# Optimization experiments

Measured on AMD Instinct MI355X. Metric: run time of the kernel, lower is better.

The kernel has to match this reference:

```python
import jax, jax.numpy as jnp
import numpy as np

B, N, D = 16, 1024, 768
H = 12
HS = D // H
L = 2  # n_ffn_layers
EPS = 1e-6


def layernorm(x, scale, bias):
    mu = jnp.mean(x, axis=-1, keepdims=True)
    var = jnp.var(x, axis=-1, keepdims=True)
    return (x - mu) * jax.lax.rsqrt(var + EPS) * scale + bias


def log_cosh(x):
    # numerically stable log(cosh(x)) = |x| + log1p(exp(-2|x|)) - log(2)
    ax = jnp.abs(x)
    return ax + jnp.log1p(jnp.exp(-2.0 * ax)) - jnp.log(2.0)


def setup_inputs() -> dict:
    key = jax.random.key(0)
    ks = jax.random.split(key, 8)
    x = jax.random.normal(ks[0], (B, N, D), dtype=jnp.float32)
    # pre-attention LayerNorm params
    ln1_scale = jnp.ones((D,), jnp.float32)
    ln1_bias = jnp.zeros((D,), jnp.float32)
    # per-head value projections [H, D, HS] (Dense, no bias)
    Wv = jax.random.normal(ks[1], (H, D, HS), jnp.float32) / np.sqrt(D)
    # per-head circulant rows alpha_delta [H, N], truncated_normal(stddev=sqrt(1/N))
    alpha = jax.random.truncated_normal(ks[2], -2.0, 2.0, (H, N), jnp.float32) * np.sqrt(1.0 / N)
    # FFN: L layers of Dense(D) + LayerNorm + swish
    Wf = jax.random.normal(ks[3], (L, D, D), jnp.float32) / np.sqrt(D)
    bf = jnp.zeros((L, D), jnp.float32)
    lnf_scale = jnp.ones((L, D), jnp.float32)
    lnf_bias = jnp.zeros((L, D), jnp.float32)
    return {"x": x, "ln1_scale": ln1_scale, "ln1_bias": ln1_bias, "Wv": Wv,
            "alpha": alpha, "Wf": Wf, "bf": bf,
            "lnf_scale": lnf_scale, "lnf_bias": lnf_bias}


def reference(x, ln1_scale, ln1_bias, Wv, alpha, Wf, bf, lnf_scale, lnf_bias):
    b, n, d = x.shape
    h, hs = Wv.shape[0], Wv.shape[2]
    # --- multi-head positional (circulant) attention on LN(x) ---
    xn = layernorm(x, ln1_scale, ln1_bias)
    v = jnp.einsum('bnd,hdk->bhnk', xn, Wv)  # per-head values
    # circulant matrix C[h, i, j] = alpha[h, (i - j) mod n]  (scipy.linalg.circulant)
    idx = (jnp.arange(n)[:, None] - jnp.arange(n)[None, :]) % n  # [n, n]
    C = alpha[:, idx]                                            # [h, n, n]
    y = jnp.einsum('hij,bhjk->bhik', C, v)                       # [b, h, n, hs]
    y = jnp.transpose(y, (0, 2, 1, 3)).reshape(b, n, h * hs)     # concat heads
    x = x + y
    # --- FFN: [Dense(D) -> LayerNorm -> swish] x L ---
    z = x
    for l in range(Wf.shape[0]):
        z = jax.nn.swish(layernorm(z @ Wf[l] + bf[l], lnf_scale[l], lnf_bias[l]))
    return log_cosh(z + x)
```

## Files before the change

### kernel.cpp

```cpp
#include <hip/hip_runtime.h>
#include <cstdint>
#include <cstddef>


typedef __attribute__((ext_vector_type(8))) short bf16x8;
typedef __attribute__((ext_vector_type(4))) float f32x4;
typedef __attribute__((ext_vector_type(4))) unsigned short us4;

__device__ __forceinline__ unsigned short f2bf(float f) {
  unsigned int u = __builtin_bit_cast(unsigned int, f);
  u += 0x7FFFu + ((u >> 16) & 1u);
  return (unsigned short)(u >> 16);
}
__device__ __forceinline__ float bf2f(unsigned short u) {
  return __builtin_bit_cast(float, (unsigned int)u << 16);
}

__device__ __forceinline__ void g2l16(const void* g, void* l) {
  __builtin_amdgcn_global_load_lds(
      (const __attribute__((address_space(1))) unsigned int*)g,
      (__attribute__((address_space(3))) unsigned int*)l,
      16, 0, 0);
}

#define BARX asm volatile("s_waitcnt lgkmcnt(0)\n\ts_barrier" ::: "memory")
#define BARV(n) asm volatile("s_waitcnt vmcnt(" #n ") lgkmcnt(0)\n\ts_barrier" ::: "memory")

__global__ __launch_bounds__(256) void pack_all(const float* __restrict__ Wv,
                                                const float* __restrict__ Wf,
                                                unsigned short* __restrict__ W2t,
                                                unsigned short* __restrict__ Wft) {
  int bid = blockIdx.x;
  if (bid < 2304) {
    int o = bid * 256 + threadIdx.x;
    int np = o / 768, d = o - np * 768;
    int h = np >> 6, k = np & 63;
    W2t[o] = f2bf(Wv[h * 49152 + d * 64 + k]);
  } else {
    int o = (bid - 2304) * 256 + threadIdx.x;
    int l = o / 589824, rem = o - l * 589824;
    int np = rem / 768, d = rem - np * 768;
    Wft[o] = f2bf(Wf[l * 589824 + d * 768 + np]);
  }
}

__device__ __forceinline__ void wave_reduce2(float& s, float& s2) {
#pragma unroll
  for (int off = 32; off > 0; off >>= 1) {
    s += __shfl_down(s, off);
    s2 += __shfl_down(s2, off);
  }
  s = __shfl(s, 0);
  s2 = __shfl(s2, 0);
}

__global__ __launch_bounds__(256) void ln1_kernel(const float* __restrict__ x,
                                                  const float* __restrict__ sc,
                                                  const float* __restrict__ bi,
                                                  unsigned short* __restrict__ out) {
  int row = blockIdx.x * 4 + (threadIdx.x >> 6);
  int lane = threadIdx.x & 63;
  size_t base = (size_t)row * 768;
  float4 v[3];
#pragma unroll
  for (int j = 0; j < 3; ++j) v[j] = *(const float4*)(x + base + lane * 4 + j * 256);
  float s = 0.f, s2 = 0.f;
#pragma unroll
  for (int j = 0; j < 3; ++j) {
    s += v[j].x + v[j].y + v[j].z + v[j].w;
    s2 += v[j].x * v[j].x + v[j].y * v[j].y + v[j].z * v[j].z + v[j].w * v[j].w;
  }
  wave_reduce2(s, s2);
  float mu = s * (1.0f / 768.0f);
  float var = s2 * (1.0f / 768.0f) - mu * mu;
  float r = rsqrtf(var + 1e-6f);
#pragma unroll
  for (int j = 0; j < 3; ++j) {
    int d = lane * 4 + j * 256;
    float4 scv = *(const float4*)(sc + d);
    float4 biv = *(const float4*)(bi + d);
    us4 o;
    o[0] = f2bf((v[j].x - mu) * r * scv.x + biv.x);
    o[1] = f2bf((v[j].y - mu) * r * scv.y + biv.y);
    o[2] = f2bf((v[j].z - mu) * r * scv.z + biv.z);
    o[3] = f2bf((v[j].w - mu) * r * scv.w + biv.w);
    *(us4*)(out + base + d) = o;
  }
}

__global__ __launch_bounds__(256) void lnswish_kernel(const unsigned short* __restrict__ g,
                                                      const float* __restrict__ sc,
                                                      const float* __restrict__ bi,
                                                      unsigned short* __restrict__ out) {
  int row = blockIdx.x * 4 + (threadIdx.x >> 6);
  int lane = threadIdx.x & 63;
  size_t base = (size_t)row * 768;
  float v[3][4];
#pragma unroll
  for (int j = 0; j < 3; ++j) {
    us4 gv = *(const us4*)(g + base + lane * 4 + j * 256);
#pragma unroll
    for (int q = 0; q < 4; ++q) v[j][q] = bf2f(gv[q]);
  }
  float s = 0.f, s2 = 0.f;
#pragma unroll
  for (int j = 0; j < 3; ++j)
#pragma unroll
    for (int q = 0; q < 4; ++q) { s += v[j][q]; s2 += v[j][q] * v[j][q]; }
  wave_reduce2(s, s2);
  float mu = s * (1.0f / 768.0f);
  float var = s2 * (1.0f / 768.0f) - mu * mu;
  float r = rsqrtf(var + 1e-6f);
#pragma unroll
  for (int j = 0; j < 3; ++j) {
    int d = lane * 4 + j * 256;
    float4 scv = *(const float4*)(sc + d);
    float4 biv = *(const float4*)(bi + d);
    const float* scp = &scv.x;
    const float* bip = &biv.x;
    us4 o;
#pragma unroll
    for (int q = 0; q < 4; ++q) {
      float z = (v[j][q] - mu) * r * scp[q] + bip[q];
      o[q] = f2bf(z / (1.0f + __expf(-z)));
    }
    *(us4*)(out + base + d) = o;
  }
}

__global__ __launch_bounds__(256) void final_kernel(const unsigned short* __restrict__ g,
                                                    const float* __restrict__ sc,
                                                    const float* __restrict__ bi,
                                                    const unsigned short* __restrict__ x2,
                                                    float* __restrict__ out) {
  int row = blockIdx.x * 4 + (threadIdx.x >> 6);
  int lane = threadIdx.x & 63;
  size_t base = (size_t)row * 768;
  float v[3][4];
#pragma unroll
  for (int j = 0; j < 3; ++j) {
    us4 gv = *(const us4*)(g + base + lane * 4 + j * 256);
#pragma unroll
    for (int q = 0; q < 4; ++q) v[j][q] = bf2f(gv[q]);
  }
  float s = 0.f, s2 = 0.f;
#pragma unroll
  for (int j = 0; j < 3; ++j)
#pragma unroll
    for (int q = 0; q < 4; ++q) { s += v[j][q]; s2 += v[j][q] * v[j][q]; }
  wave_reduce2(s, s2);
  float mu = s * (1.0f / 768.0f);
  float var = s2 * (1.0f / 768.0f) - mu * mu;
  float r = rsqrtf(var + 1e-6f);
#pragma unroll
  for (int j = 0; j < 3; ++j) {
    int d = lane * 4 + j * 256;
    float4 scv = *(const float4*)(sc + d);
    float4 biv = *(const float4*)(bi + d);
    us4 xv = *(const us4*)(x2 + base + d);
    const float* scp = &scv.x;
    const float* bip = &biv.x;
    float4 o;
    float* op = &o.x;
#pragma unroll
    for (int q = 0; q < 4; ++q) {
      float z = (v[j][q] - mu) * r * scp[q] + bip[q];
      float sw = z / (1.0f + __expf(-z));
      float t = sw + bf2f(xv[q]);
      float ax = fabsf(t);
      op[q] = ax + __logf(1.0f + __expf(-2.0f * ax)) - 0.69314718055994531f;
    }
    *(float4*)(out + base + d) = o;
  }
}

template <int K>
__device__ __forceinline__ void gemm256(const unsigned short* __restrict__ A,
                                        const unsigned short* __restrict__ Bt,
                                        int m0, int n0, unsigned short* lds,
                                        f32x4 acc[8][4]) {
  const int tid = threadIdx.x;
  const int lane = tid & 63;
  const int wid = tid >> 6;
  const int wm = (wid >> 2) << 6;
  const int wn = (wid & 3) << 5;
  const int fm = lane & 15, fq = lane >> 4;
  const int srow = tid >> 3;
  const int sslot = (tid & 7) ^ (srow & 7);
  const size_t abase = (size_t)(m0 + srow) * K + (sslot << 3);
  const size_t bbase = (size_t)(n0 + srow) * K + (sslot << 3);

  bf16x8 aq[4][2], bq[4][2];

#define STG_A(kt, bb, c)                                                     \
  g2l16(A + abase + (size_t)((c) << 6) * K + ((kt) << 6),                    \
        lds + ((bb) << 15) + ((c) << 12) + (tid << 3))
#define STG_B(kt, bb, c)                                                     \
  g2l16(Bt + bbase + (size_t)((c) << 6) * K + ((kt) << 6),                   \
        lds + ((bb) << 15) + 16384 + ((c) << 12) + (tid << 3))
#define LDA(bb, mh)                                                          \
  _Pragma("unroll") for (int mt = 0; mt < 4; ++mt) {                         \
    const unsigned short* p =                                                \
        lds + ((bb) << 15) + (wm + ((mh) << 7) + (mt << 4) + fm) * 64;       \
    _Pragma("unroll") for (int kk = 0; kk < 2; ++kk)                         \
      aq[mt][kk] = *(const bf16x8*)(p + ((((kk << 2) + fq) ^ (fm & 7)) << 3)); \
  }
#define LDB(bb, nh)                                                          \
  _Pragma("unroll") for (int nt = 0; nt < 2; ++nt) {                         \
    const unsigned short* p = lds + ((bb) << 15) + 16384 +                   \
                              (wn + ((nh) << 7) + (nt << 4) + fm) * 64;      \
    _Pragma("unroll") for (int kk = 0; kk < 2; ++kk)                         \
      bq[((nh) << 1) + nt][kk] =                                             \
          *(const bf16x8*)(p + ((((kk << 2) + fq) ^ (fm & 7)) << 3));        \
  }
#define MMX(mh, nh)                                                          \
  {                                                                          \
    __builtin_amdgcn_s_setprio(1);                                           \
    _Pragma("unroll") for (int mt = 0; mt < 4; ++mt)                         \
    _Pragma("unroll") for (int nt = 0; nt < 2; ++nt)                         \
    _Pragma("unroll") for (int kk = 0; kk < 2; ++kk)                         \
      acc[((mh) << 2) + mt][((nh) << 1) + nt] =                              \
          __builtin_amdgcn_mfma_f32_16x16x32_bf16(                           \
              aq[mt][kk], bq[((nh) << 1) + nt][kk],                          \
              acc[((mh) << 2) + mt][((nh) << 1) + nt], 0, 0, 0);             \
    __builtin_amdgcn_s_setprio(0);                                           \
  }

  constexpr int NT = K >> 6;
  STG_A(0, 0, 0); STG_A(0, 0, 1); STG_A(0, 0, 2); STG_A(0, 0, 3);
  STG_B(0, 0, 0); STG_B(0, 0, 1); STG_B(0, 0, 2); STG_B(0, 0, 3);
  STG_A(1, 1, 0); STG_A(1, 1, 1);
  STG_B(1, 1, 0); STG_B(1, 1, 1);
  BARV(4);

  for (int t = 0; t < (NT >> 1) - 1; ++t) {
    const int k1 = 2 * t + 1, k2 = 2 * t + 2, k3 = 2 * t + 3;
    LDA(0, 0); LDB(0, 0);
    STG_A(k1, 1, 2); STG_A(k1, 1, 3);
    MMX(0, 0); BARX;
    LDB(0, 1);
    STG_B(k1, 1, 2); STG_B(k1, 1, 3);
    MMX(0, 1); BARX;
    LDA(0, 1);
    STG_A(k2, 0, 0); STG_A(k2, 0, 1);
    MMX(1, 0); BARX;
    STG_B(k2, 0, 0); STG_B(k2, 0, 1);
    MMX(1, 1); BARV(4);
    LDA(1, 0); LDB(1, 0);
    STG_A(k2, 0, 2); STG_A(k2, 0, 3);
    MMX(0, 0); BARX;
    LDB(1, 1);
    STG_B(k2, 0, 2); STG_B(k2, 0, 3);
    MMX(0, 1); BARX;
    LDA(1, 1);
    STG_A(k3, 1, 0); STG_A(k3, 1, 1);
    MMX(1, 0); BARX;
    STG_B(k3, 1, 0); STG_B(k3, 1, 1);
    MMX(1, 1); BARV(4);
  }
  {
    const int k1 = NT - 1;
    LDA(0, 0); LDB(0, 0);
    STG_A(k1, 1, 2); STG_A(k1, 1, 3);
    MMX(0, 0); BARX;
    LDB(0, 1);
    STG_B(k1, 1, 2); STG_B(k1, 1, 3);
    MMX(0, 1); BARX;
    LDA(0, 1);
    MMX(1, 0); BARX;
    MMX(1, 1);
    BARV(0);
    LDA(1, 0); LDB(1, 0);
    MMX(0, 0); BARX;
    LDB(1, 1);
    MMX(0, 1); BARX;
    LDA(1, 1);
    MMX(1, 0); BARX;
    MMX(1, 1);
  }
#undef STG_A
#undef STG_B
#undef LDA
#undef LDB
#undef MMX
}

__device__ __forceinline__ void decode256(int bid, int& m0, int& n0) {
  int wg = (bid & 7) * 24 + (bid >> 3);
  int mi = wg / 3, ni = wg - mi * 3;
  m0 = mi << 8;
  n0 = ni << 8;
}

__global__ __launch_bounds__(512, 2) void gemm1_256(const unsigned short* __restrict__ A,
                                                    const unsigned short* __restrict__ W2t,
                                                    unsigned short* __restrict__ Vt) {
  extern __shared__ unsigned short lds[];
  f32x4 acc[8][4] = {};
  int m0, n0;
  decode256(blockIdx.x, m0, n0);
  gemm256<768>(A, W2t, m0, n0, lds, acc);
  const int lane = threadIdx.x & 63, wid = threadIdx.x >> 6;
  const int wm = (wid >> 2) << 6, wn = (wid & 3) << 5;
  const int fm = lane & 15, fq = lane >> 4;
#pragma unroll
  for (int ai = 0; ai < 8; ++ai) {
    int rowb = m0 + wm + ((ai >> 2) << 7) + ((ai & 3) << 4) + (fq << 2);
    int b = rowb >> 10, n = rowb & 1023;
#pragma unroll
    for (int nj = 0; nj < 4; ++nj) {
      int col = n0 + wn + ((nj >> 1) << 7) + ((nj & 1) << 4) + fm;
      int h = col >> 6, ck = col & 63;
      size_t off = ((size_t)h << 20) + (size_t)((b << 6) + ck) * 1024 + n;
      us4 v;
#pragma unroll
      for (int r = 0; r < 4; ++r) v[r] = f2bf(acc[ai][nj][r]);
      *(us4*)(Vt + off) = v;
    }
  }
}

__global__ __launch_bounds__(512, 2) void gemmf_256(const unsigned short* __restrict__ A,
                                                    const unsigned short* __restrict__ Bt,
                                                    const float* __restrict__ bias,
                                                    unsigned short* __restrict__ g) {
  extern __shared__ unsigned short lds[];
  f32x4 acc[8][4] = {};
  int m0, n0;
  decode256(blockIdx.x, m0, n0);
  gemm256<768>(A, Bt, m0, n0, lds, acc);
  const int lane = threadIdx.x & 63, wid = threadIdx.x >> 6;
  const int wm = (wid >> 2) << 6, wn = (wid & 3) << 5;
  const int fm = lane & 15, fq = lane >> 4;
#pragma unroll
  for (int ai = 0; ai < 8; ++ai) {
    int rowb = m0 + wm + ((ai >> 2) << 7) + ((ai & 3) << 4) + (fq << 2);
#pragma unroll
    for (int nj = 0; nj < 4; ++nj) {
      int col = n0 + wn + ((nj >> 1) << 7) + ((nj & 1) << 4) + fm;
      float bc = bias[col];
#pragma unroll
      for (int r = 0; r < 4; ++r)
        g[(size_t)(rowb + r) * 768 + col] = f2bf(acc[ai][nj][r] + bc);
    }
  }
}

__global__ __launch_bounds__(512, 2) void circ256_kernel(const float* __restrict__ alpha,
                                                         const unsigned short* __restrict__ Vt,
                                                         const float* __restrict__ xin,
                                                         unsigned short* __restrict__ x2bf) {
  extern __shared__ unsigned short lds[];
  unsigned short* sAc = lds;
  unsigned short* sB = lds + 10304;
  f32x4 acc[8][4] = {};

  int wg = (blockIdx.x & 7) * 24 + (blockIdx.x >> 3);
  int h = wg >> 4, tt = wg & 15;
  int m0 = (tt >> 2) << 8, n0 = (tt & 3) << 8;

  const int tid = threadIdx.x;
  const int lane = tid & 63, wid = tid >> 6;
  const int wm = (wid >> 2) << 6, wn = (wid & 3) << 5;
  const int fm = lane & 15, fq = lane >> 4;
  const int srow = tid >> 3;
  const int sslot = (tid & 7) ^ (srow & 7);

  const float* ah = alpha + (h << 10);
#pragma unroll
  for (int c = 0; c < 8; ++c)
    for (int u = tid; u < 1280; u += 512)
      sAc[c * 1288 + u] = f2bf(ah[(m0 - 769 - u - c) & 1023]);

  const unsigned short* Bt = Vt + ((size_t)h << 20);
  const size_t bbase = (size_t)(n0 + srow) * 1024 + (sslot << 3);

  bf16x8 aq[4][2], bq[4][2];

#define CSTG(kt, bb, c)                                                      \
  g2l16(Bt + bbase + (size_t)((c) << 6) * 1024 + ((kt) << 6),                \
        sB + ((bb) << 14) + ((c) << 12) + (tid << 3))
#define CLDA(kt, mh)                                                         \
  _Pragma("unroll") for (int mt = 0; mt < 4; ++mt)                           \
  _Pragma("unroll") for (int kk = 0; kk < 2; ++kk) {                         \
    int d_ = ((kt) << 6) + (kk << 5) + (fq << 3) + 255 -                     \
             (wm + ((mh) << 7) + (mt << 4) + fm);                            \
    int c_ = d_ & 7;                                                         \
    aq[mt][kk] = *(const bf16x8*)(sAc + c_ * 1288 + (d_ - c_));              \
  }
#define CLDB(bb, nh)                                                         \
  _Pragma("unroll") for (int nt = 0; nt < 2; ++nt) {                         \
    const unsigned short* p =                                                \
        sB + ((bb) << 14) + (wn + ((nh) << 7) + (nt << 4) + fm) * 64;        \
    _Pragma("unroll") for (int kk = 0; kk < 2; ++kk)                         \
      bq[((nh) << 1) + nt][kk] =                                             \
          *(const bf16x8*)(p + ((((kk << 2) + fq) ^ (fm & 7)) << 3));        \
  }
#define CMMX(mh, nh)                                                         \
  {                                                                          \
    __builtin_amdgcn_s_setprio(1);                                           \
    _Pragma("unroll") for (int mt = 0; mt < 4; ++mt)                         \
    _Pragma("unroll") for (int nt = 0; nt < 2; ++nt)                         \
    _Pragma("unroll") for (int kk = 0; kk < 2; ++kk)                         \
      acc[((mh) << 2) + mt][((nh) << 1) + nt] =                              \
          __builtin_amdgcn_mfma_f32_16x16x32_bf16(                           \
              aq[mt][kk], bq[((nh) << 1) + nt][kk],                          \
              acc[((mh) << 2) + mt][((nh) << 1) + nt], 0, 0, 0);             \
    __builtin_amdgcn_s_setprio(0);                                           \
  }

  CSTG(0, 0, 0); CSTG(0, 0, 1); CSTG(0, 0, 2); CSTG(0, 0, 3);
  CSTG(1, 1, 0); CSTG(1, 1, 1);
  BARV(2);

  for (int it = 0; it < 7; ++it) {
    const int k0 = 2 * it, k1 = 2 * it + 1, k2 = 2 * it + 2, k3 = 2 * it + 3;
    CLDA(k0, 0); CLDB(0, 0);
    CSTG(k1, 1, 2);
    CMMX(0, 0); BARX;
    CLDB(0, 1);
    CSTG(k1, 1, 3);
    CMMX(0, 1); BARX;
    CLDA(k0, 1);
    CSTG(k2, 0, 0);
    CMMX(1, 0); BARX;
    CSTG(k2, 0, 1);
    CMMX(1, 1); BARV(2);
    CLDA(k1, 0); CLDB(1, 0);
    CSTG(k2, 0, 2);
    CMMX(0, 0); BARX;
    CLDB(1, 1);
    CSTG(k2, 0, 3);
    CMMX(0, 1); BARX;
    CLDA(k1, 1);
    CSTG(k3, 1, 0);
    CMMX(1, 0); BARX;
    CSTG(k3, 1, 1);
    CMMX(1, 1); BARV(2);
  }
  CLDA(14, 0); CLDB(0, 0);
  CSTG(15, 1, 2);
  CMMX(0, 0); BARX;
  CLDB(0, 1);
  CSTG(15, 1, 3);
  CMMX(0, 1); BARX;
  CLDA(14, 1);
  CMMX(1, 0); BARX;
  CMMX(1, 1);
  BARV(0);
  CLDA(15, 0); CLDB(1, 0);
  CMMX(0, 0); BARX;
  CLDB(1, 1);
  CMMX(0, 1); BARX;
  CLDA(15, 1);
  CMMX(1, 0); BARX;
  CMMX(1, 1);
#undef CSTG
#undef CLDA
#undef CLDB
#undef CMMX

#pragma unroll
  for (int ai = 0; ai < 8; ++ai) {
    int i = m0 + wm + ((ai >> 2) << 7) + ((ai & 3) << 4) + (fq << 2);
#pragma unroll
    for (int nj = 0; nj < 4; ++nj) {
      int col = n0 + wn + ((nj >> 1) << 7) + ((nj & 1) << 4) + fm;
      int b = col >> 6, k = col & 63;
      size_t off = ((size_t)(b << 10) + i) * 768 + (h << 6) + k;
#pragma unroll
      for (int r = 0; r < 4; ++r) {
        float val = acc[ai][nj][r] + xin[off + (size_t)r * 768];
        x2bf[off + (size_t)r * 768] = f2bf(val);
      }
    }
  }
}

extern "C" void kernel_launch(void* const* d_in, const int* in_sizes, int n_in,
                              void* d_out, int out_size, void* d_ws, size_t ws_size,
                              hipStream_t stream) {
  const float* x = (const float*)d_in[0];
  const float* ln1_s = (const float*)d_in[1];
  const float* ln1_b = (const float*)d_in[2];
  const float* Wv = (const float*)d_in[3];
  const float* alpha = (const float*)d_in[4];
  const float* Wf = (const float*)d_in[5];
  const float* bf = (const float*)d_in[6];
  const float* lnf_s = (const float*)d_in[7];
  const float* lnf_b = (const float*)d_in[8];
  float* out = (float*)d_out;

  char* ws = (char*)d_ws;
  unsigned short* slotA = (unsigned short*)ws;
  unsigned short* Vt = (unsigned short*)(ws + 25165824);
  unsigned short* gbf = Vt;
  unsigned short* slotX = (unsigned short*)(ws + 50331648);
  unsigned short* W2t = (unsigned short*)(ws + 75497472);
  unsigned short* Wft = (unsigned short*)(ws + 76677120);

  hipFuncSetAttribute((const void*)gemm1_256,
                      hipFuncAttributeMaxDynamicSharedMemorySize, 131072);
  hipFuncSetAttribute((const void*)gemmf_256,
                      hipFuncAttributeMaxDynamicSharedMemorySize, 131072);
  hipFuncSetAttribute((const void*)circ256_kernel,
                      hipFuncAttributeMaxDynamicSharedMemorySize, 86144);

  pack_all<<<6912, 256, 0, stream>>>(Wv, Wf, W2t, Wft);

  ln1_kernel<<<4096, 256, 0, stream>>>(x, ln1_s, ln1_b, slotA);
  gemm1_256<<<192, 512, 131072, stream>>>(slotA, W2t, Vt);
  circ256_kernel<<<192, 512, 86144, stream>>>(alpha, Vt, x, slotX);
  gemmf_256<<<192, 512, 131072, stream>>>(slotX, Wft, bf, gbf);
  lnswish_kernel<<<4096, 256, 0, stream>>>(gbf, lnf_s, lnf_b, slotA);
  gemmf_256<<<192, 512, 131072, stream>>>(slotA, Wft + 589824, bf + 768, gbf);
  final_kernel<<<4096, 256, 0, stream>>>(gbf, lnf_s + 768, lnf_b + 768, slotX, out);
}
```

Before: 270.3 us.

## Fuse second FFN GEMM with LayerNorm, swish, residual and log-cosh epilogue

Replaces the last gemmf_256 plus final_kernel pair with one kernel that computes 64-row by full-768-column output tiles. Owning whole rows lets it do the LayerNorm reduction in-block through shuffles and LDS, then apply swish, the residual add and log_cosh before writing fp32 output. This removes the bf16 round trip of the GEMM result and one launch. In exchange it uses a new 256-block grid with a shallower two-stage pipeline. The epilogue's scalar column-strided stores and residual loads may also coalesce less well.

Result: slower. 277.9 us (+2.8%).

```diff
diff --git a/kernel.cpp b/kernel.cpp
--- a/kernel.cpp
+++ b/kernel.cpp
@@ -23,6 +23,7 @@
       16, 0, 0);
 }
 
+#define WAITB(n) asm volatile("s_waitcnt vmcnt(" #n ") lgkmcnt(0)\n\ts_barrier" ::: "memory")
 #define BARX asm volatile("s_waitcnt lgkmcnt(0)\n\ts_barrier" ::: "memory")
 #define BARV(n) asm volatile("s_waitcnt vmcnt(" #n ") lgkmcnt(0)\n\ts_barrier" ::: "memory")
 
@@ -125,52 +126,6 @@
       o[q] = f2bf(z / (1.0f + __expf(-z)));
     }
     *(us4*)(out + base + d) = o;
-  }
-}
-
-__global__ __launch_bounds__(256) void final_kernel(const unsigned short* __restrict__ g,
-                                                    const float* __restrict__ sc,
-                                                    const float* __restrict__ bi,
-                                                    const unsigned short* __restrict__ x2,
-                                                    float* __restrict__ out) {
-  int row = blockIdx.x * 4 + (threadIdx.x >> 6);
-  int lane = threadIdx.x & 63;
-  size_t base = (size_t)row * 768;
-  float v[3][4];
-#pragma unroll
-  for (int j = 0; j < 3; ++j) {
-    us4 gv = *(const us4*)(g + base + lane * 4 + j * 256);
-#pragma unroll
-    for (int q = 0; q < 4; ++q) v[j][q] = bf2f(gv[q]);
-  }
-  float s = 0.f, s2 = 0.f;
-#pragma unroll
-  for (int j = 0; j < 3; ++j)
-#pragma unroll
-    for (int q = 0; q < 4; ++q) { s += v[j][q]; s2 += v[j][q] * v[j][q]; }
-  wave_reduce2(s, s2);
-  float mu = s * (1.0f / 768.0f);
-  float var = s2 * (1.0f / 768.0f) - mu * mu;
-  float r = rsqrtf(var + 1e-6f);
-#pragma unroll
-  for (int j = 0; j < 3; ++j) {
-    int d = lane * 4 + j * 256;
-    float4 scv = *(const float4*)(sc + d);
-    float4 biv = *(const float4*)(bi + d);
-    us4 xv = *(const us4*)(x2 + base + d);
-    const float* scp = &scv.x;
-    const float* bip = &biv.x;
-    float4 o;
-    float* op = &o.x;
-#pragma unroll
-    for (int q = 0; q < 4; ++q) {
-      float z = (v[j][q] - mu) * r * scp[q] + bip[q];
-      float sw = z / (1.0f + __expf(-z));
-      float t = sw + bf2f(xv[q]);
-      float ax = fabsf(t);
-      op[q] = ax + __logf(1.0f + __expf(-2.0f * ax)) - 0.69314718055994531f;
-    }
-    *(float4*)(out + base + d) = o;
   }
 }
 
@@ -477,6 +432,161 @@
   }
 }
 
+__global__ __launch_bounds__(512, 2) void gemmf_ln1(
+    const unsigned short* __restrict__ A,
+    const unsigned short* __restrict__ Wt,
+    const float* __restrict__ bias,
+    const float* __restrict__ sc,
+    const float* __restrict__ bi,
+    const unsigned short* __restrict__ x2,
+    float* __restrict__ outp) {
+  extern __shared__ unsigned short lds[];
+  unsigned short* sA = lds;
+  unsigned short* sB = lds + 4096;
+  float* fst = (float*)lds;
+
+  f32x4 acc[4][6] = {};
+  int bid = blockIdx.x;
+  int p = ((bid & 7) << 5) + (bid >> 3);
+  const int m0 = p << 6;
+
+  const int tid = threadIdx.x;
+  const int lane = tid & 63;
+  const int wid = tid >> 6;
+  const int fm = lane & 15, fq = lane >> 4;
+  const int wc0 = wid * 96;
+  const int brow = tid >> 2;
+  const int cg = tid & 3;
+  const size_t wbase = (size_t)brow * 768 + ((cg ^ ((brow >> 1) & 3)) << 3);
+  const int t2 = tid & 255;
+  const int ar = t2 >> 2;
+  const size_t abase = (size_t)(m0 + ar) * 768 + ((cg ^ ((ar >> 1) & 3)) << 3);
+
+#define FSTG(step, buf)                                                      \
+  {                                                                          \
+    int k0_ = (step) << 5;                                                   \
+    _Pragma("unroll") for (int c = 0; c < 6; ++c)                            \
+      g2l16(Wt + wbase + c * 98304 + k0_,                                    \
+            sB + (buf) * 24576 + c * 4096 + (tid << 3));                     \
+    g2l16(A + abase + k0_, sA + (buf) * 2048 + (t2 << 3));                   \
+  }
+#define FCOMP(buf)                                                           \
+  {                                                                          \
+    bf16x8 aq[4], bq[6];                                                     \
+    _Pragma("unroll") for (int mt = 0; mt < 4; ++mt) {                       \
+      int ra = (mt << 4) + fm;                                               \
+      aq[mt] = *(const bf16x8*)(sA + (buf) * 2048 + (ra << 5) +              \
+                                ((fq ^ ((ra >> 1) & 3)) << 3));              \
+    }                                                                        \
+    _Pragma("unroll") for (int nt = 0; nt < 6; ++nt) {                       \
+      int rb = wc0 + (nt << 4) + fm;                                         \
+      bq[nt] = *(const bf16x8*)(sB + (buf) * 24576 + (rb << 5) +             \
+                                ((fq ^ ((rb >> 1) & 3)) << 3));              \
+    }                                                                        \
+    __builtin_amdgcn_s_setprio(1);                                           \
+    _Pragma("unroll") for (int mt = 0; mt < 4; ++mt)                         \
+    _Pragma("unroll") for (int nt = 0; nt < 6; ++nt)                         \
+      acc[mt][nt] = __builtin_amdgcn_mfma_f32_16x16x32_bf16(                 \
+          aq[mt], bq[nt], acc[mt][nt], 0, 0, 0);                             \
+    __builtin_amdgcn_s_setprio(0);                                           \
+  }
+
+  FSTG(0, 0);
+  for (int it = 0; it < 24; ++it) {
+    WAITB(0);
+    if (it < 23) FSTG(it + 1, (it + 1) & 1);
+    FCOMP(it & 1);
+  }
+  __syncthreads();
+
+  float bc[6];
+#pragma unroll
+  for (int nt = 0; nt < 6; ++nt) bc[nt] = bias[wc0 + (nt << 4) + fm];
+#pragma unroll
+  for (int mt = 0; mt < 4; ++mt)
+#pragma unroll
+    for (int nt = 0; nt < 6; ++nt)
+#pragma unroll
+      for (int r = 0; r < 4; ++r) acc[mt][nt][r] += bc[nt];
+
+  float s[4][4], s2[4][4];
+#pragma unroll
+  for (int mt = 0; mt < 4; ++mt)
+#pragma unroll
+    for (int r = 0; r < 4; ++r) {
+      float a = 0.f, b2 = 0.f;
+#pragma unroll
+      for (int nt = 0; nt < 6; ++nt) {
+        float v = acc[mt][nt][r];
+        a += v;
+        b2 += v * v;
+      }
+      s[mt][r] = a;
+      s2[mt][r] = b2;
+    }
+#pragma unroll
+  for (int off = 1; off <= 8; off <<= 1)
+#pragma unroll
+    for (int mt = 0; mt < 4; ++mt)
+#pragma unroll
+      for (int r = 0; r < 4; ++r) {
+        s[mt][r] += __shfl_xor(s[mt][r], off);
+        s2[mt][r] += __shfl_xor(s2[mt][r], off);
+      }
+  if (fm == 0) {
+#pragma unroll
+    for (int mt = 0; mt < 4; ++mt)
+#pragma unroll
+      for (int r = 0; r < 4; ++r) {
+        int row = (mt << 4) + (fq << 2) + r;
+        fst[wid * 64 + row] = s[mt][r];
+        fst[512 + wid * 64 + row] = s2[mt][r];
+      }
+  }
+  __syncthreads();
+  if (tid < 64) {
+    float ts = 0.f, ts2 = 0.f;
+#pragma unroll
+    for (int w = 0; w < 8; ++w) {
+      ts += fst[w * 64 + tid];
+      ts2 += fst[512 + w * 64 + tid];
+    }
+    float mu = ts * (1.0f / 768.0f);
+    float var = ts2 * (1.0f / 768.0f) - mu * mu;
+    fst[1024 + tid] = mu;
+    fst[1088 + tid] = rsqrtf(var + 1e-6f);
+  }
+  __syncthreads();
+
+  float scv[6], biv[6];
+#pragma unroll
+  for (int nt = 0; nt < 6; ++nt) {
+    scv[nt] = sc[wc0 + (nt << 4) + fm];
+    biv[nt] = bi[wc0 + (nt << 4) + fm];
+  }
+#pragma unroll
+  for (int mt = 0; mt < 4; ++mt)
+#pragma unroll
+    for (int r = 0; r < 4; ++r) {
+      int row = (mt << 4) + (fq << 2) + r;
+      float mu = fst[1024 + row];
+      float rr = fst[1088 + row];
+      size_t rg = (size_t)(m0 + row) * 768;
+#pragma unroll
+      for (int nt = 0; nt < 6; ++nt) {
+        int col = wc0 + (nt << 4) + fm;
+        float z = (acc[mt][nt][r] - mu) * rr * scv[nt] + biv[nt];
+        float sw = z / (1.0f + __expf(-z));
+        float t = sw + bf2f(x2[rg + col]);
+        float ax = fabsf(t);
+        outp[rg + col] =
+            ax + __logf(1.0f + __expf(-2.0f * ax)) - 0.69314718055994531f;
+      }
+    }
+#undef FSTG
+#undef FCOMP
+}
+
 extern "C" void kernel_launch(void* const* d_in, const int* in_sizes, int n_in,
                               void* d_out, int out_size, void* d_ws, size_t ws_size,
                               hipStream_t stream) {
@@ -505,6 +615,8 @@
                       hipFuncAttributeMaxDynamicSharedMemorySize, 131072);
   hipFuncSetAttribute((const void*)circ256_kernel,
                       hipFuncAttributeMaxDynamicSharedMemorySize, 86144);
+  hipFuncSetAttribute((const void*)gemmf_ln1,
+                      hipFuncAttributeMaxDynamicSharedMemorySize, 106496);
 
   pack_all<<<6912, 256, 0, stream>>>(Wv, Wf, W2t, Wft);
 
@@ -513,6 +625,7 @@
   circ256_kernel<<<192, 512, 86144, stream>>>(alpha, Vt, x, slotX);
   gemmf_256<<<192, 512, 131072, stream>>>(slotX, Wft, bf, gbf);
   lnswish_kernel<<<4096, 256, 0, stream>>>(gbf, lnf_s, lnf_b, slotA);
-  gemmf_256<<<192, 512, 131072, stream>>>(slotA, Wft + 589824, bf + 768, gbf);
-  final_kernel<<<4096, 256, 0, stream>>>(gbf, lnf_s + 768, lnf_b + 768, slotX, out);
-}
+  gemmf_ln1<<<256, 512, 106496, stream>>>(slotA, Wft + 589824, bf + 768,
+                                          lnf_s + 768, lnf_b + 768, slotX,
+                                          out);
+}
```
